# Optimization experiments

Measured on AMD Instinct MI355X. Metric: run time of the kernel, lower is better.

The kernel has to match this reference:

```python
import jax, jax.numpy as jnp
import numpy as np

PH = PW = 5  # roi_size
EPS = 1e-5


def _conv1x1(x, w, b):
    # x: (B,Cin,H,W), w: (Cout,Cin)
    return jnp.einsum('bchw,oc->bohw', x, w) + b[None, :, None, None]


def _resize_ac(x, oh, ow):
    # F.interpolate bilinear, align_corners=True. x: (B,C,H,W)
    B, C, H, W = x.shape
    ys = jnp.linspace(0.0, H - 1.0, oh)
    xs = jnp.linspace(0.0, W - 1.0, ow)
    y0 = jnp.floor(ys).astype(jnp.int32); y1 = jnp.minimum(y0 + 1, H - 1)
    x0 = jnp.floor(xs).astype(jnp.int32); x1 = jnp.minimum(x0 + 1, W - 1)
    ly = (ys - y0)[:, None]; lx = (xs - x0)[None, :]
    v00 = x[:, :, y0[:, None], x0[None, :]]
    v01 = x[:, :, y0[:, None], x1[None, :]]
    v10 = x[:, :, y1[:, None], x0[None, :]]
    v11 = x[:, :, y1[:, None], x1[None, :]]
    return v00 * (1 - ly) * (1 - lx) + v01 * (1 - ly) * lx + v10 * ly * (1 - lx) + v11 * ly * lx


def _roi_align_one(feat, box):
    # torchvision RoIAlign, spatial_scale=1, sampling_ratio=1, aligned=False
    # feat: (C,H,W), box: (x1,y1,x2,y2)
    C, H, W = feat.shape
    bx1, by1, bx2, by2 = box[0], box[1], box[2], box[3]
    rw = jnp.maximum(bx2 - bx1, 1.0)
    rh = jnp.maximum(by2 - by1, 1.0)
    xs = bx1 + (jnp.arange(PW, dtype=feat.dtype) + 0.5) * (rw / PW)
    ys = by1 + (jnp.arange(PH, dtype=feat.dtype) + 0.5) * (rh / PH)
    yg = jnp.broadcast_to(ys[:, None], (PH, PW))
    xg = jnp.broadcast_to(xs[None, :], (PH, PW))
    valid = (yg >= -1.0) & (yg <= H) & (xg >= -1.0) & (xg <= W)
    y = jnp.clip(yg, 0.0, H - 1.0); x = jnp.clip(xg, 0.0, W - 1.0)
    y0 = jnp.floor(y).astype(jnp.int32); x0 = jnp.floor(x).astype(jnp.int32)
    y1i = jnp.minimum(y0 + 1, H - 1); x1i = jnp.minimum(x0 + 1, W - 1)
    ly = y - y0; lx = x - x0
    v = (feat[:, y0, x0] * (1 - ly) * (1 - lx) + feat[:, y0, x1i] * (1 - ly) * lx
         + feat[:, y1i, x0] * ly * (1 - lx) + feat[:, y1i, x1i] * ly * lx)
    return v * valid  # (C,PH,PW)


def _layernorm(x, w, b):
    mu = jnp.mean(x, -1, keepdims=True)
    var = jnp.var(x, -1, keepdims=True)
    return (x - mu) * jax.lax.rsqrt(var + EPS) * w + b


def setup_inputs() -> dict:
    key = jax.random.key(0)
    ks = jax.random.split(key, 16)
    B, G, NB, HF = 8, 8, 16, 28
    x4 = jax.random.normal(ks[0], (B, 1024, 14, 14), jnp.float32)
    x5 = jax.random.normal(ks[1], (B, 2048, 7, 7), jnp.float32)
    bx = jax.random.uniform(ks[2], (B, NB), minval=0.0, maxval=18.0)
    by = jax.random.uniform(ks[3], (B, NB), minval=0.0, maxval=18.0)
    bw = jax.random.uniform(ks[4], (B, NB), minval=3.0, maxval=10.0)
    bh = jax.random.uniform(ks[5], (B, NB), minval=3.0, maxval=10.0)
    boxes = jnp.stack([bx, by, jnp.minimum(bx + bw, 28.0), jnp.minimum(by + bh, 28.0)], -1)
    group = jax.random.randint(ks[6], (B, G, 2), 0, NB, jnp.int32)
    real_in_num = jnp.full((B,), G, jnp.int32)
    label_s = jax.random.randint(ks[7], (B, G), 0, 6, jnp.int64)
    label_s = jnp.where(jnp.arange(G)[None, :] % 3 == 0, -1, label_s)  # exercise both branches
    skeleton = jax.random.normal(ks[8], (B, G, HF, HF), jnp.float32)
    D = 1536 * PH * PW  # 38400
    return {
        'x4': x4, 'x5': x5, 'boxes': boxes, 'skeleton': skeleton,
        'group': group, 'real_in_num': real_in_num, 'label_s': label_s,
        'conv1_w': jax.random.normal(ks[9], (), jnp.float32) * 0.5,
        'conv1_b': jax.random.normal(ks[10], (), jnp.float32) * 0.1,
        'conv2_w': jax.random.normal(ks[11], (512, 1024), jnp.float32) * 0.03,
        'conv2_b': jnp.zeros((512,), jnp.float32),
        'conv3_w': jax.random.normal(ks[12], (1024, 2048), jnp.float32) * 0.02,
        'conv3_b': jnp.zeros((1024,), jnp.float32),
        'norm1_w': jnp.ones((D,), jnp.float32), 'norm1_b': jnp.zeros((D,), jnp.float32),
        'norm2_w': jnp.ones((512,), jnp.float32), 'norm2_b': jnp.zeros((512,), jnp.float32),
        'fc1_w': jax.random.normal(ks[13], (512, D), jnp.float32) * float(np.sqrt(2.0 / D)),
        'fc1_b': jnp.zeros((512,), jnp.float32),
        'fc2_w': jax.random.normal(ks[14], (6, 512), jnp.float32) * float(np.sqrt(2.0 / 512)),
        'fc2_b': jnp.zeros((6,), jnp.float32),
    }


def reference(x4, x5, boxes, skeleton, group, real_in_num, label_s,
              conv1_w, conv1_b, conv2_w, conv2_b, conv3_w, conv3_b,
              norm1_w, norm1_b, norm2_w, norm2_b, fc1_w, fc1_b, fc2_w, fc2_b):
    B, G = skeleton.shape[0], skeleton.shape[1]
    HF, WF = skeleton.shape[2], skeleton.shape[3]
    # backbone heads: 1x1 conv + bilinear upsample (align_corners=True), concat
    f4 = _resize_ac(_conv1x1(x4, conv2_w, conv2_b), HF, WF)   # (B,512,28,28)
    f5 = _resize_ac(_conv1x1(x5, conv3_w, conv3_b), HF, WF)   # (B,1024,28,28)
    app = jnp.concatenate([f4, f5], axis=1)                   # (B,1536,28,28)
    C = app.shape[1]
    # per-person pose gate: 1x1 conv (scalar on single channel) + sigmoid
    gate = jax.nn.sigmoid(skeleton * conv1_w + conv1_b)       # (B,G,28,28)
    gated = gate[:, :, None] * app[:, None]                   # (B,G,C,28,28)
    use_gate = (label_s != -1)[:, :, None, None, None]
    pose_feature = jnp.where(use_gate, gated, app[:, None])   # (B,G,C,28,28)
    # union box of the two interacting people (get_box_tensor)
    bidx = jnp.arange(B)[:, None]
    b1 = boxes[bidx, group[..., 0]]                           # (B,G,4)
    b2 = boxes[bidx, group[..., 1]]
    ub = jnp.stack([jnp.minimum(b1[..., 0], b2[..., 0]), jnp.minimum(b1[..., 1], b2[..., 1]),
                    jnp.maximum(b1[..., 2], b2[..., 2]), jnp.maximum(b1[..., 3], b2[..., 3])], -1)
    # batched RoIAlign over all N = B*G boxes
    feats = pose_feature.reshape(B * G, C, HF, WF)
    rois = jax.vmap(_roi_align_one)(feats, ub.reshape(B * G, 4))  # (N,C,5,5)
    sk = rois.reshape(B * G, -1)                              # (N,38400)
    sk = jax.nn.relu(_layernorm(sk, norm1_w, norm1_b))
    # dropout(p=0.9) is identity in eval mode
    sk = sk @ fc1_w.T + fc1_b
    sk = _layernorm(sk, norm2_w, norm2_b)
    score = sk @ fc2_w.T + fc2_b                              # (N,6)
    return score
```

## Files before the change

kernel.cpp:

```cpp
#include <hip/hip_runtime.h>
#include <math.h>

#define B8   8
#define HW4  196
#define HW5  49
#define HFW  28
#define NPIX 784
#define CAPP 1536
#define D1   38400
#define NR   64

typedef short short8 __attribute__((ext_vector_type(8)));
typedef short short4v __attribute__((ext_vector_type(4)));
typedef float floatx16 __attribute__((ext_vector_type(16)));

__device__ __forceinline__ unsigned short f2bf(float f) {
  unsigned u = __float_as_uint(f);
  u += 0x7FFF + ((u >> 16) & 1);
  return (unsigned short)(u >> 16);
}

struct Params {
  const float *x4, *x5, *boxes, *skel;
  const int *group, *label;
  const float *c1w, *c1b, *w2c, *b2c, *w3c, *b3c;
  const float *n1w, *n1b, *n2w, *n2b, *fw1, *fb1, *fw2, *fb2;
  float* out;
  unsigned short *x4T, *x5T, *sknT;
  float *f4T, *f5T, *tap4w, *tap5w, *descw, *roisP, *stats, *out1;
  int *tap4o, *tap5o, *desco;
};

union SharedU {
  float tile[32 * 201];
  struct {
    unsigned short As[2][4096];
    unsigned short Bs[2][4096];
  } g;
  struct {
    float cw4[16], cw5[16], wgs;
    int co4[16], co5[16];
    float red[8];
  } roi;
  struct {
    float red[8];
    float red2[24];
  } ln;
};

__device__ __forceinline__ void gemm_unit(
    SharedU& sh, const unsigned short* __restrict__ A, const float* __restrict__ Bw,
    float* __restrict__ C, int mt, int nt, int k0, int kchunk,
    int K, int N, int Mvalid, bool accum) {
  int t = threadIdx.x;
  int wave = t >> 6, lane = t & 63;
  int wm = wave & 1, wn = wave >> 1;
  const unsigned short* Aptr = A + (size_t)(mt * 64) * K + k0;
  const float* Bptr = Bw + (size_t)(nt * 64) * K + k0;

  int m0 = t >> 3, ka = (t & 7) * 8, koa = t & 7;
  int n0 = t >> 4, kbo = (t & 15) * 4, kob = (t & 15) >> 1, half = t & 1;

  short8 areg[2][2];
  float4 breg[2][4];
  floatx16 acc;
#pragma unroll
  for (int i = 0; i < 16; i++) acc[i] = 0.f;
  int nkb = kchunk >> 6;

  auto LOAD = [&](int s, int j) {
    int kof = j * 64;
    areg[s][0] = *(const short8*)(Aptr + (size_t)m0 * K + kof + ka);
    areg[s][1] = *(const short8*)(Aptr + (size_t)(m0 + 32) * K + kof + ka);
#pragma unroll
    for (int i = 0; i < 4; i++)
      breg[s][i] = *(const float4*)(Bptr + (size_t)(n0 + 16 * i) * K + kof + kbo);
  };
  auto STORE = [&](int buf, int s) {
    *(short8*)&sh.g.As[buf][koa * 512 + ((m0 ^ koa)) * 8] = areg[s][0];
    *(short8*)&sh.g.As[buf][koa * 512 + (((m0 + 32) ^ koa)) * 8] = areg[s][1];
#pragma unroll
    for (int i = 0; i < 4; i++) {
      short4v v;
      v[0] = (short)f2bf(breg[s][i].x); v[1] = (short)f2bf(breg[s][i].y);
      v[2] = (short)f2bf(breg[s][i].z); v[3] = (short)f2bf(breg[s][i].w);
      int n = n0 + 16 * i;
      *(short4v*)&sh.g.Bs[buf][kob * 512 + ((n ^ kob)) * 8 + half * 4] = v;
    }
  };

  LOAD(0, 0);
  STORE(0, 0);
  if (nkb > 1) LOAD(1, 1);
  __syncthreads();

  for (int kb = 0; kb < nkb; kb++) {
    int buf = kb & 1;
    if (kb + 2 < nkb) LOAD(buf, kb + 2);
#pragma unroll
    for (int s = 0; s < 4; s++) {
      int ko = 2 * s + (lane >> 5);
      int am = wm * 32 + (lane & 31);
      int bn = wn * 32 + (lane & 31);
      short8 af = *(const short8*)&sh.g.As[buf][ko * 512 + ((am ^ ko)) * 8];
      short8 bf = *(const short8*)&sh.g.Bs[buf][ko * 512 + ((bn ^ ko)) * 8];
      acc = __builtin_amdgcn_mfma_f32_32x32x16_bf16(af, bf, acc, 0, 0, 0);
    }
    if (kb + 1 < nkb) STORE(1 - buf, (kb + 1) & 1);
    __syncthreads();
  }

  int col = nt * 64 + wn * 32 + (lane & 31);
  int rbase = mt * 64 + wm * 32 + 4 * (lane >> 5);
  if (accum) {
#pragma unroll
    for (int reg = 0; reg < 16; reg++) {
      int row = rbase + (reg & 3) + 8 * (reg >> 2);
      if (row < Mvalid) atomicAdd(&C[(size_t)row * N + col], acc[reg]);
    }
  } else {
#pragma unroll
    for (int reg = 0; reg < 16; reg++) {
      int row = rbase + (reg & 3) + 8 * (reg >> 2);
      if (row < Mvalid) C[(size_t)row * N + col] = acc[reg];
    }
  }
}

__device__ __forceinline__ float gate_val(const float* sk, int yy, int xx,
                                          float c1w, float c1b, bool use) {
  if (!use) return 1.f;
  float z = sk[yy * HFW + xx] * c1w + c1b;
  return 1.f / (1.f + expf(-z));
}

__device__ void run_phase0(const Params& p, SharedU& sh) {
  int bid = blockIdx.x, t = threadIdx.x, gb = gridDim.x;
  int gtid = bid * 256 + t;
  int nth = gb * 256;
  float4 z4 = make_float4(0.f, 0.f, 0.f, 0.f);
  for (int i = gtid; i < 319488; i += nth) ((float4*)p.f4T)[i] = z4;
  for (int i = gtid; i < 8192; i += nth) ((float4*)p.out1)[i] = z4;
  if (gtid < 128) p.stats[gtid] = 0.f;

  for (int u = bid; u < 836; u += gb) {
    __syncthreads();
    if (u < 256) {
      int b = u >> 5, cc = u & 31;
      for (int i = t; i < 32 * HW4; i += 256) {
        int c = i / HW4, hw = i - c * HW4;
        sh.tile[c * 201 + hw] = p.x4[((size_t)(b * 1024 + cc * 32 + c)) * HW4 + hw];
      }
      __syncthreads();
      for (int i = t; i < HW4 * 32; i += 256) {
        int hw = i >> 5, c = i & 31;
        p.x4T[((size_t)(b * HW4 + hw)) * 1024 + cc * 32 + c] = f2bf(sh.tile[c * 201 + hw]);
      }
    } else if (u < 768) {
      int u2 = u - 256;
      int b = u2 >> 6, cc = u2 & 63;
      for (int i = t; i < 32 * HW5; i += 256) {
        int c = i / HW5, hw = i - c * HW5;
        sh.tile[c * 51 + hw] = p.x5[((size_t)(b * 2048 + cc * 32 + c)) * HW5 + hw];
      }
      __syncthreads();
      for (int i = t; i < HW5 * 32; i += 256) {
        int hw = i >> 5, c = i & 31;
        p.x5T[((size_t)(b * HW5 + hw)) * 2048 + cc * 32 + c] = f2bf(sh.tile[c * 51 + hw]);
      }
    } else if (u < 832) {
      int bg = u - 768;
      if (t < 25) {
        int b = bg >> 3;
        int i1 = p.group[bg * 2 + 0], i2 = p.group[bg * 2 + 1];
        const float* bb1 = p.boxes + (size_t)(b * 16 + i1) * 4;
        const float* bb2 = p.boxes + (size_t)(b * 16 + i2) * 4;
        float ux1 = fminf(bb1[0], bb2[0]);
        float uy1 = fminf(bb1[1], bb2[1]);
        float ux2 = fmaxf(bb1[2], bb2[2]);
        float uy2 = fmaxf(bb1[3], bb2[3]);
        float rw = fmaxf(ux2 - ux1, 1.0f), rh = fmaxf(uy2 - uy1, 1.0f);
        int iy = t / 5, ix = t % 5;
        float sy = uy1 + (iy + 0.5f) * (rh * 0.2f);
        float sx = ux1 + (ix + 0.5f) * (rw * 0.2f);
        float valid = (sy >= -1.0f && sy <= 28.0f && sx >= -1.0f && sx <= 28.0f) ? 1.f : 0.f;
        float y = fminf(fmaxf(sy, 0.f), 27.f);
        float x = fminf(fmaxf(sx, 0.f), 27.f);
        int y0 = (int)floorf(y), x0 = (int)floorf(x);
        int y1 = min(y0 + 1, 27), x1 = min(x0 + 1, 27);
        float ly = y - (float)y0, lx = x - (float)x0;
        bool use = (p.label[bg] != -1);
        float c1w = p.c1w[0], c1b = p.c1b[0];
        const float* sk = p.skel + (size_t)bg * NPIX;
        int idx = (bg * 25 + t) * 4;
        p.descw[idx + 0] = (1.f - ly) * (1.f - lx) * valid * gate_val(sk, y0, x0, c1w, c1b, use);
        p.descw[idx + 1] = (1.f - ly) * lx * valid * gate_val(sk, y0, x1, c1w, c1b, use);
        p.descw[idx + 2] = ly * (1.f - lx) * valid * gate_val(sk, y1, x0, c1w, c1b, use);
        p.descw[idx + 3] = ly * lx * valid * gate_val(sk, y1, x1, c1w, c1b, use);
        p.desco[idx + 0] = y0 * HFW + x0;
        p.desco[idx + 1] = y0 * HFW + x1;
        p.desco[idx + 2] = y1 * HFW + x0;
        p.desco[idx + 3] = y1 * HFW + x1;
      }
    } else {
      int pix = (u - 832) * 196 + t;
      if (t < 196) {
        int y = pix / HFW, x = pix % HFW;
        {
          float sy = y * (13.0f / 27.0f), sx = x * (13.0f / 27.0f);
          int y0 = (int)sy, x0 = (int)sx;
          int y1 = min(y0 + 1, 13), x1 = min(x0 + 1, 13);
          float ly = sy - y0, lx = sx - x0;
          p.tap4o[pix * 4 + 0] = y0 * 14 + x0; p.tap4w[pix * 4 + 0] = (1.f - ly) * (1.f - lx);
          p.tap4o[pix * 4 + 1] = y0 * 14 + x1; p.tap4w[pix * 4 + 1] = (1.f - ly) * lx;
          p.tap4o[pix * 4 + 2] = y1 * 14 + x0; p.tap4w[pix * 4 + 2] = ly * (1.f - lx);
          p.tap4o[pix * 4 + 3] = y1 * 14 + x1; p.tap4w[pix * 4 + 3] = ly * lx;
        }
        {
          float sy = y * (6.0f / 27.0f), sx = x * (6.0f / 27.0f);
          int y0 = (int)sy, x0 = (int)sx;
          int y1 = min(y0 + 1, 6), x1 = min(x0 + 1, 6);
          float ly = sy - y0, lx = sx - x0;
          p.tap5o[pix * 4 + 0] = y0 * 7 + x0; p.tap5w[pix * 4 + 0] = (1.f - ly) * (1.f - lx);
          p.tap5o[pix * 4 + 1] = y0 * 7 + x1; p.tap5w[pix * 4 + 1] = (1.f - ly) * lx;
          p.tap5o[pix * 4 + 2] = y1 * 7 + x0; p.tap5w[pix * 4 + 2] = ly * (1.f - lx);
          p.tap5o[pix * 4 + 3] = y1 * 7 + x1; p.tap5w[pix * 4 + 3] = ly * lx;
        }
      }
    }
  }
}

__device__ void run_phase1(const Params& p, SharedU& sh) {
  int bid = blockIdx.x, gb = gridDim.x;
  for (int u = bid; u < 1696; u += gb) {
    __syncthreads();
    if (u < 800) {
      int mt = u % 25, r = u / 25;
      int nt = r & 7, sp = r >> 3;
      gemm_unit(sh, p.x4T, p.w2c, p.f4T, mt, nt, sp * 256, 256, 1024, 512, 1568, true);
    } else {
      int u2 = u - 800;
      int mt = u2 % 7, r = u2 / 7;
      int nt = r & 15, sp = r >> 4;
      gemm_unit(sh, p.x5T, p.w3c, p.f5T, mt, nt, sp * 256, 256, 2048, 1024, 392, true);
    }
  }
}

__device__ void run_phase2(const Params& p, SharedU& sh) {
  int bid = blockIdx.x, t = threadIdx.x, gb = gridDim.x;
  for (int u = bid; u < 1600; u += gb) {
    __syncthreads();
    int pp = u % 25, bg = u / 25, b = bg >> 3;
    int di = (bg * 25 + pp) * 4;
    if (t < 16) {
      int i = t >> 2, j = t & 3;
      float wg = p.descw[di + i];
      int pix = p.desco[di + i];
      sh.roi.cw4[t] = wg * p.tap4w[pix * 4 + j];
      sh.roi.co4[t] = (b * HW4 + p.tap4o[pix * 4 + j]) * 512;
      sh.roi.cw5[t] = wg * p.tap5w[pix * 4 + j];
      sh.roi.co5[t] = (b * HW5 + p.tap5o[pix * 4 + j]) * 1024;
    }
    if (t == 16) sh.roi.wgs = p.descw[di] + p.descw[di + 1] + p.descw[di + 2] + p.descw[di + 3];
    __syncthreads();
    float w4r[16], w5r[16];
    int o4r[16], o5r[16];
    float wg = sh.roi.wgs;
#pragma unroll
    for (int i = 0; i < 16; i++) {
      w4r[i] = sh.roi.cw4[i]; o4r[i] = sh.roi.co4[i];
      w5r[i] = sh.roi.cw5[i]; o5r[i] = sh.roi.co5[i];
    }
    float ls = 0.f, ls2 = 0.f;
    float* outp = p.roisP + (size_t)(bg * 25 + pp) * CAPP;
    for (int c = t; c < 512; c += 256) {
      float acc = wg * p.b2c[c];
#pragma unroll
      for (int i = 0; i < 16; i++) acc = fmaf(w4r[i], p.f4T[o4r[i] + c], acc);
      outp[c] = acc;
      ls += acc; ls2 = fmaf(acc, acc, ls2);
    }
    for (int c = t; c < 1024; c += 256) {
      float acc = wg * p.b3c[c];
#pragma unroll
      for (int i = 0; i < 16; i++) acc = fmaf(w5r[i], p.f5T[o5r[i] + c], acc);
      outp[512 + c] = acc;
      ls += acc; ls2 = fmaf(acc, acc, ls2);
    }
    for (int off = 32; off; off >>= 1) {
      ls += __shfl_down(ls, off);
      ls2 += __shfl_down(ls2, off);
    }
    int wv = t >> 6;
    if ((t & 63) == 0) { sh.roi.red[wv] = ls; sh.roi.red[4 + wv] = ls2; }
    __syncthreads();
    if (t == 0) {
      atomicAdd(&p.stats[bg * 2 + 0], sh.roi.red[0] + sh.roi.red[1] + sh.roi.red[2] + sh.roi.red[3]);
      atomicAdd(&p.stats[bg * 2 + 1], sh.roi.red[4] + sh.roi.red[5] + sh.roi.red[6] + sh.roi.red[7]);
    }
  }
}

__device__ void run_phase3(const Params& p, SharedU& sh) {
  int bid = blockIdx.x, t = threadIdx.x, gb = gridDim.x;
  for (int u = bid; u < 384; u += gb) {
    __syncthreads();
    int r = u / 6, ch = u - r * 6;
    int c0 = ch * 256;
    float S = p.stats[r * 2], S2 = p.stats[r * 2 + 1];
    float mu = S * (1.f / D1);
    float var = S2 * (1.f / D1) - mu * mu;
    float rs = rsqrtf(var + 1e-5f);
    const float* rp = p.roisP + (size_t)r * 25 * CAPP + c0;
#pragma unroll
    for (int pp = 0; pp < 25; pp++)
      sh.tile[pp * 257 + t] = rp[(size_t)pp * CAPP + t];
    __syncthreads();
    unsigned short* op = p.sknT + (size_t)r * D1 + c0 * 25;
    const float* wv = p.n1w + c0 * 25;
    const float* bv = p.n1b + c0 * 25;
    for (int j = t; j < 6400; j += 256) {
      unsigned cc = (unsigned)j / 25u;
      unsigned pp = (unsigned)j - cc * 25u;
      float x = sh.tile[pp * 257 + cc];
      float v = fmaf((x - mu) * rs, wv[j], bv[j]);
      op[j] = f2bf(fmaxf(v, 0.f));
    }
  }
}

__device__ void run_phase4(const Params& p, SharedU& sh) {
  int bid = blockIdx.x, gb = gridDim.x;
  for (int u = bid; u < 960; u += gb) {
    __syncthreads();
    int nt = u & 7, sp = u >> 3;
    gemm_unit(sh, p.sknT, p.fw1, p.out1, 0, nt, sp * 320, 320, 38400, 512, 64, true);
  }
}

__device__ void run_phase5(const Params& p, SharedU& sh) {
  int bid = blockIdx.x, t = threadIdx.x, gb = gridDim.x;
  for (int r = bid; r < NR; r += gb) {
    __syncthreads();
    int j1 = t, j2 = t + 256;
    float v1 = p.out1[r * 512 + j1] + p.fb1[j1];
    float v2 = p.out1[r * 512 + j2] + p.fb1[j2];
    float s = v1 + v2, s2 = v1 * v1 + v2 * v2;
    for (int off = 32; off; off >>= 1) {
      s += __shfl_down(s, off);
      s2 += __shfl_down(s2, off);
    }
    int wv = t >> 6;
    if ((t & 63) == 0) { sh.ln.red[wv] = s; sh.ln.red[4 + wv] = s2; }
    __syncthreads();
    float S = sh.ln.red[0] + sh.ln.red[1] + sh.ln.red[2] + sh.ln.red[3];
    float S2 = sh.ln.red[4] + sh.ln.red[5] + sh.ln.red[6] + sh.ln.red[7];
    float mu = S / 512.f;
    float var = S2 / 512.f - mu * mu;
    float rs = rsqrtf(var + 1e-5f);
    float n1v = fmaf((v1 - mu) * rs, p.n2w[j1], p.n2b[j1]);
    float n2v = fmaf((v2 - mu) * rs, p.n2w[j2], p.n2b[j2]);
    float pm[6];
#pragma unroll
    for (int m = 0; m < 6; m++)
      pm[m] = n1v * p.fw2[m * 512 + j1] + n2v * p.fw2[m * 512 + j2];
#pragma unroll
    for (int m = 0; m < 6; m++)
      for (int off = 32; off; off >>= 1) pm[m] += __shfl_down(pm[m], off);
    if ((t & 63) == 0) {
#pragma unroll
      for (int m = 0; m < 6; m++) sh.ln.red2[wv * 6 + m] = pm[m];
    }
    __syncthreads();
    if (t < 6)
      p.out[r * 6 + t] = sh.ln.red2[t] + sh.ln.red2[6 + t] + sh.ln.red2[12 + t] +
                         sh.ln.red2[18 + t] + p.fb2[t];
  }
}

__global__ __launch_bounds__(256, 4) void k_phase0(Params p) { __shared__ SharedU sh; run_phase0(p, sh); }
__global__ __launch_bounds__(256, 4) void k_phase1(Params p) { __shared__ SharedU sh; run_phase1(p, sh); }
__global__ __launch_bounds__(256, 4) void k_phase2(Params p) { __shared__ SharedU sh; run_phase2(p, sh); }
__global__ __launch_bounds__(256, 4) void k_phase3(Params p) { __shared__ SharedU sh; run_phase3(p, sh); }
__global__ __launch_bounds__(256, 4) void k_phase4(Params p) { __shared__ SharedU sh; run_phase4(p, sh); }
__global__ __launch_bounds__(256, 4) void k_phase5(Params p) { __shared__ SharedU sh; run_phase5(p, sh); }

extern "C" void kernel_launch(void* const* d_in, const int* in_sizes, int n_in,
                              void* d_out, int out_size, void* d_ws, size_t ws_size,
                              hipStream_t stream) {
  Params p;
  p.x4    = (const float*)d_in[0];
  p.x5    = (const float*)d_in[1];
  p.boxes = (const float*)d_in[2];
  p.skel  = (const float*)d_in[3];
  p.group = (const int*)d_in[4];
  p.label = (const int*)d_in[6];
  p.c1w   = (const float*)d_in[7];
  p.c1b   = (const float*)d_in[8];
  p.w2c   = (const float*)d_in[9];
  p.b2c   = (const float*)d_in[10];
  p.w3c   = (const float*)d_in[11];
  p.b3c   = (const float*)d_in[12];
  p.n1w   = (const float*)d_in[13];
  p.n1b   = (const float*)d_in[14];
  p.n2w   = (const float*)d_in[15];
  p.n2b   = (const float*)d_in[16];
  p.fw1   = (const float*)d_in[17];
  p.fb1   = (const float*)d_in[18];
  p.fw2   = (const float*)d_in[19];
  p.fb2   = (const float*)d_in[20];
  p.out   = (float*)d_out;

  float* ws = (float*)d_ws;
  p.x4T   = (unsigned short*)ws;
  p.x5T   = (unsigned short*)(ws + 819200);
  p.f4T   = ws + 1277952;
  p.f5T   = ws + 2097152;
  p.tap4w = ws + 2555904;
  p.tap4o = (int*)(ws + 2559040);
  p.tap5w = ws + 2562176;
  p.tap5o = (int*)(ws + 2565312);
  p.descw = ws + 2568448;
  p.desco = (int*)(ws + 2574848);
  p.roisP = ws + 2581248;
  p.stats = ws + 5038848;
  p.sknT  = (unsigned short*)(ws + 5038976);
  p.out1  = ws + 6267776;

  k_phase0<<<836,  256, 0, stream>>>(p);
  k_phase1<<<1696, 256, 0, stream>>>(p);
  k_phase2<<<1600, 256, 0, stream>>>(p);
  k_phase3<<<384,  256, 0, stream>>>(p);
  k_phase4<<<960,  256, 0, stream>>>(p);
  k_phase5<<<64,   256, 0, stream>>>(p);
}
```

Before: 249.6 us.

## Give each phase kernel its own shared layout and single-buffer GEMM for occupancy

Replaces the shared-memory union with per-kernel structs so each phase kernel allocates only the LDS it needs. The GEMM tile loop moves from double-buffered LDS with two-stage register prefetch to a single LDS buffer with one-stage prefetch, halving LDS and register use for the GEMM. Launch bounds for the GEMM, RoI and final kernels are raised to 8 blocks per CU. The cost is an extra barrier per k-step and less overlap of global loads with MFMA work, which more resident blocks must make up for. The grid size in the unseen launch code may also need to match.

```diff
diff --git a/kernel.cpp b/kernel.cpp
--- a/kernel.cpp
+++ b/kernel.cpp
@@ -31,25 +31,21 @@
   int *tap4o, *tap5o, *desco;
 };
 
-union SharedU {
-  float tile[32 * 201];
-  struct {
-    unsigned short As[2][4096];
-    unsigned short Bs[2][4096];
-  } g;
-  struct {
-    float cw4[16], cw5[16], wgs;
-    int co4[16], co5[16];
-    float red[8];
-  } roi;
-  struct {
-    float red[8];
-    float red2[24];
-  } ln;
+struct Sh0 { float tile[6432]; };
+struct GemmSh {
+  unsigned short As[4096];
+  unsigned short Bs[4096];
 };
+struct Sh2 {
+  float cw4[16], cw5[16], wgs;
+  int co4[16], co5[16];
+  float red[8];
+};
+struct Sh3 { float tile[6424]; };
+struct Sh5 { float red[8]; float red2[24]; };
 
 __device__ __forceinline__ void gemm_unit(
-    SharedU& sh, const unsigned short* __restrict__ A, const float* __restrict__ Bw,
+    GemmSh& sh, const unsigned short* __restrict__ A, const float* __restrict__ Bw,
     float* __restrict__ C, int mt, int nt, int k0, int kchunk,
     int K, int N, int Mvalid, bool accum) {
   int t = threadIdx.x;
@@ -61,53 +57,55 @@
   int m0 = t >> 3, ka = (t & 7) * 8, koa = t & 7;
   int n0 = t >> 4, kbo = (t & 15) * 4, kob = (t & 15) >> 1, half = t & 1;
 
-  short8 areg[2][2];
-  float4 breg[2][4];
+  short8 areg[2];
+  float4 breg[4];
   floatx16 acc;
 #pragma unroll
   for (int i = 0; i < 16; i++) acc[i] = 0.f;
   int nkb = kchunk >> 6;
 
-  auto LOAD = [&](int s, int j) {
+  auto LOAD = [&](int j) {
     int kof = j * 64;
-    areg[s][0] = *(const short8*)(Aptr + (size_t)m0 * K + kof + ka);
-    areg[s][1] = *(const short8*)(Aptr + (size_t)(m0 + 32) * K + kof + ka);
+    areg[0] = *(const short8*)(Aptr + (size_t)m0 * K + kof + ka);
+    areg[1] = *(const short8*)(Aptr + (size_t)(m0 + 32) * K + kof + ka);
 #pragma unroll
     for (int i = 0; i < 4; i++)
-      breg[s][i] = *(const float4*)(Bptr + (size_t)(n0 + 16 * i) * K + kof + kbo);
+      breg[i] = *(const float4*)(Bptr + (size_t)(n0 + 16 * i) * K + kof + kbo);
   };
-  auto STORE = [&](int buf, int s) {
-    *(short8*)&sh.g.As[buf][koa * 512 + ((m0 ^ koa)) * 8] = areg[s][0];
-    *(short8*)&sh.g.As[buf][koa * 512 + (((m0 + 32) ^ koa)) * 8] = areg[s][1];
+  auto STORE = [&]() {
+    *(short8*)&sh.As[koa * 512 + ((m0 ^ koa)) * 8] = areg[0];
+    *(short8*)&sh.As[koa * 512 + (((m0 + 32) ^ koa)) * 8] = areg[1];
 #pragma unroll
     for (int i = 0; i < 4; i++) {
       short4v v;
-      v[0] = (short)f2bf(breg[s][i].x); v[1] = (short)f2bf(breg[s][i].y);
-      v[2] = (short)f2bf(breg[s][i].z); v[3] = (short)f2bf(breg[s][i].w);
+      v[0] = (short)f2bf(breg[i].x); v[1] = (short)f2bf(breg[i].y);
+      v[2] = (short)f2bf(breg[i].z); v[3] = (short)f2bf(breg[i].w);
       int n = n0 + 16 * i;
-      *(short4v*)&sh.g.Bs[buf][kob * 512 + ((n ^ kob)) * 8 + half * 4] = v;
+      *(short4v*)&sh.Bs[kob * 512 + ((n ^ kob)) * 8 + half * 4] = v;
     }
   };
 
-  LOAD(0, 0);
-  STORE(0, 0);
-  if (nkb > 1) LOAD(1, 1);
+  LOAD(0);
+  STORE();
   __syncthreads();
 
   for (int kb = 0; kb < nkb; kb++) {
-    int buf = kb & 1;
-    if (kb + 2 < nkb) LOAD(buf, kb + 2);
+    bool more = (kb + 1) < nkb;
+    if (more) LOAD(kb + 1);
 #pragma unroll
     for (int s = 0; s < 4; s++) {
       int ko = 2 * s + (lane >> 5);
       int am = wm * 32 + (lane & 31);
       int bn = wn * 32 + (lane & 31);
-      short8 af = *(const short8*)&sh.g.As[buf][ko * 512 + ((am ^ ko)) * 8];
-      short8 bf = *(const short8*)&sh.g.Bs[buf][ko * 512 + ((bn ^ ko)) * 8];
+      short8 af = *(const short8*)&sh.As[ko * 512 + ((am ^ ko)) * 8];
+      short8 bf = *(const short8*)&sh.Bs[ko * 512 + ((bn ^ ko)) * 8];
       acc = __builtin_amdgcn_mfma_f32_32x32x16_bf16(af, bf, acc, 0, 0, 0);
     }
-    if (kb + 1 < nkb) STORE(1 - buf, (kb + 1) & 1);
-    __syncthreads();
+    __syncthreads();
+    if (more) {
+      STORE();
+      __syncthreads();
+    }
   }
 
   int col = nt * 64 + wn * 32 + (lane & 31);
@@ -134,7 +132,8 @@
   return 1.f / (1.f + expf(-z));
 }
 
-__device__ void run_phase0(const Params& p, SharedU& sh) {
+__global__ __launch_bounds__(256, 4) void k_phase0(Params p) {
+  __shared__ Sh0 sh;
   int bid = blockIdx.x, t = threadIdx.x, gb = gridDim.x;
   int gtid = bid * 256 + t;
   int nth = gb * 256;
@@ -231,7 +230,8 @@
   }
 }
 
-__device__ void run_phase1(const Params& p, SharedU& sh) {
+__global__ __launch_bounds__(256, 8) void k_phase1(Params p) {
+  __shared__ GemmSh sh;
   int bid = blockIdx.x, gb = gridDim.x;
   for (int u = bid; u < 1696; u += gb) {
     __syncthreads();
@@ -248,7 +248,8 @@
   }
 }
 
-__device__ void run_phase2(const Params& p, SharedU& sh) {
+__global__ __launch_bounds__(256, 8) void k_phase2(Params p) {
+  __shared__ Sh2 sh;
   int bid = blockIdx.x, t = threadIdx.x, gb = gridDim.x;
   for (int u = bid; u < 1600; u += gb) {
     __syncthreads();
@@ -258,20 +259,20 @@
       int i = t >> 2, j = t & 3;
       float wg = p.descw[di + i];
       int pix = p.desco[di + i];
-      sh.roi.cw4[t] = wg * p.tap4w[pix * 4 + j];
-      sh.roi.co4[t] = (b * HW4 + p.tap4o[pix * 4 + j]) * 512;
-      sh.roi.cw5[t] = wg * p.tap5w[pix * 4 + j];
-      sh.roi.co5[t] = (b * HW5 + p.tap5o[pix * 4 + j]) * 1024;
-    }
-    if (t == 16) sh.roi.wgs = p.descw[di] + p.descw[di + 1] + p.descw[di + 2] + p.descw[di + 3];
+      sh.cw4[t] = wg * p.tap4w[pix * 4 + j];
+      sh.co4[t] = (b * HW4 + p.tap4o[pix * 4 + j]) * 512;
+      sh.cw5[t] = wg * p.tap5w[pix * 4 + j];
+      sh.co5[t] = (b * HW5 + p.tap5o[pix * 4 + j]) * 1024;
+    }
+    if (t == 16) sh.wgs = p.descw[di] + p.descw[di + 1] + p.descw[di + 2] + p.descw[di + 3];
     __syncthreads();
     float w4r[16], w5r[16];
     int o4r[16], o5r[16];
-    float wg = sh.roi.wgs;
+    float wg = sh.wgs;
 #pragma unroll
     for (int i = 0; i < 16; i++) {
-      w4r[i] = sh.roi.cw4[i]; o4r[i] = sh.roi.co4[i];
-      w5r[i] = sh.roi.cw5[i]; o5r[i] = sh.roi.co5[i];
+      w4r[i] = sh.cw4[i]; o4r[i] = sh.co4[i];
+      w5r[i] = sh.cw5[i]; o5r[i] = sh.co5[i];
     }
     float ls = 0.f, ls2 = 0.f;
     float* outp = p.roisP + (size_t)(bg * 25 + pp) * CAPP;
@@ -294,16 +295,17 @@
       ls2 += __shfl_down(ls2, off);
     }
     int wv = t >> 6;
-    if ((t & 63) == 0) { sh.roi.red[wv] = ls; sh.roi.red[4 + wv] = ls2; }
+    if ((t & 63) == 0) { sh.red[wv] = ls; sh.red[4 + wv] = ls2; }
     __syncthreads();
     if (t == 0) {
-      atomicAdd(&p.stats[bg * 2 + 0], sh.roi.red[0] + sh.roi.red[1] + sh.roi.red[2] + sh.roi.red[3]);
-      atomicAdd(&p.stats[bg * 2 + 1], sh.roi.red[4] + sh.roi.red[5] + sh.roi.red[6] + sh.roi.red[7]);
-    }
-  }
-}
-
-__device__ void run_phase3(const Params& p, SharedU& sh) {
+      atomicAdd(&p.stats[bg * 2 + 0], sh.red[0] + sh.red[1] + sh.red[2] + sh.red[3]);
+      atomicAdd(&p.stats[bg * 2 + 1], sh.red[4] + sh.red[5] + sh.red[6] + sh.red[7]);
+    }
+  }
+}
+
+__global__ __launch_bounds__(256, 4) void k_phase3(Params p) {
+  __shared__ Sh3 sh;
   int bid = blockIdx.x, t = threadIdx.x, gb = gridDim.x;
   for (int u = bid; u < 384; u += gb) {
     __syncthreads();
@@ -331,7 +333,8 @@
   }
 }
 
-__device__ void run_phase4(const Params& p, SharedU& sh) {
+__global__ __launch_bounds__(256, 8) void k_phase4(Params p) {
+  __shared__ GemmSh sh;
   int bid = blockIdx.x, gb = gridDim.x;
   for (int u = bid; u < 960; u += gb) {
     __syncthreads();
@@ -340,7 +343,8 @@
   }
 }
 
-__device__ void run_phase5(const Params& p, SharedU& sh) {
+__global__ __launch_bounds__(256, 8) void k_phase5(Params p) {
+  __shared__ Sh5 sh;
   int bid = blockIdx.x, t = threadIdx.x, gb = gridDim.x;
   for (int r = bid; r < NR; r += gb) {
     __syncthreads();
@@ -353,10 +357,10 @@
       s2 += __shfl_down(s2, off);
     }
     int wv = t >> 6;
-    if ((t & 63) == 0) { sh.ln.red[wv] = s; sh.ln.red[4 + wv] = s2; }
-    __syncthreads();
-    float S = sh.ln.red[0] + sh.ln.red[1] + sh.ln.red[2] + sh.ln.red[3];
-    float S2 = sh.ln.red[4] + sh.ln.red[5] + sh.ln.red[6] + sh.ln.red[7];
+    if ((t & 63) == 0) { sh.red[wv] = s; sh.red[4 + wv] = s2; }
+    __syncthreads();
+    float S = sh.red[0] + sh.red[1] + sh.red[2] + sh.red[3];
+    float S2 = sh.red[4] + sh.red[5] + sh.red[6] + sh.red[7];
     float mu = S / 512.f;
     float var = S2 / 512.f - mu * mu;
     float rs = rsqrtf(var + 1e-5f);
@@ -371,21 +375,14 @@
       for (int off = 32; off; off >>= 1) pm[m] += __shfl_down(pm[m], off);
     if ((t & 63) == 0) {
 #pragma unroll
-      for (int m = 0; m < 6; m++) sh.ln.red2[wv * 6 + m] = pm[m];
+      for (int m = 0; m < 6; m++) sh.red2[wv * 6 + m] = pm[m];
     }
     __syncthreads();
     if (t < 6)
-      p.out[r * 6 + t] = sh.ln.red2[t] + sh.ln.red2[6 + t] + sh.ln.red2[12 + t] +
-                         sh.ln.red2[18 + t] + p.fb2[t];
-  }
-}
-
-__global__ __launch_bounds__(256, 4) void k_phase0(Params p) { __shared__ SharedU sh; run_phase0(p, sh); }
-__global__ __launch_bounds__(256, 4) void k_phase1(Params p) { __shared__ SharedU sh; run_phase1(p, sh); }
-__global__ __launch_bounds__(256, 4) void k_phase2(Params p) { __shared__ SharedU sh; run_phase2(p, sh); }
-__global__ __launch_bounds__(256, 4) void k_phase3(Params p) { __shared__ SharedU sh; run_phase3(p, sh); }
-__global__ __launch_bounds__(256, 4) void k_phase4(Params p) { __shared__ SharedU sh; run_phase4(p, sh); }
-__global__ __launch_bounds__(256, 4) void k_phase5(Params p) { __shared__ SharedU sh; run_phase5(p, sh); }
+      p.out[r * 6 + t] = sh.red2[t] + sh.red2[6 + t] + sh.red2[12 + t] +
+                         sh.red2[18 + t] + p.fb2[t];
+  }
+}
 
 extern "C" void kernel_launch(void* const* d_in, const int* in_sizes, int n_in,
                               void* d_out, int out_size, void* d_ws, size_t ws_size,
```

New measurement: 302.0 us. +21.0%, slower.
